# Kernel optimization log

Hardware: AMD Instinct MI355X
Metric: run time of the kernel (lower is better)

Reference implementation:

```python
import math
import jax, jax.numpy as jnp
import numpy as np

NUM_EXPERTS = 8
TOP_K = 2
CAPACITY_FACTOR = 1.0
B, S, H, I = 4, 2048, 1024, 4096


def setup_inputs() -> dict:
    key = jax.random.key(0)
    k_x, k_rw, k_wi, k_wo = jax.random.split(key, 4)
    x = jax.random.normal(k_x, (B, S, H), dtype=jnp.float32)
    # router: nn.Linear(H, E), xavier_uniform weight, zero-ish bias
    lim = math.sqrt(6.0 / (H + NUM_EXPERTS))
    router_w = jax.random.uniform(k_rw, (NUM_EXPERTS, H), minval=-lim, maxval=lim, dtype=jnp.float32)
    router_b = jnp.zeros((NUM_EXPERTS,), dtype=jnp.float32)
    # expert weights (scaled randn for numerical sanity)
    experts_inter = jax.random.normal(k_wi, (NUM_EXPERTS - 1, H, I), dtype=jnp.float32) / math.sqrt(H)
    experts_out = jax.random.normal(k_wo, (NUM_EXPERTS - 1, I, H), dtype=jnp.float32) / math.sqrt(I)
    return {"x": x, "router_w": router_w, "router_b": router_b,
            "experts_inter": experts_inter, "experts_out": experts_out}


def reference(x, router_w, router_b, experts_inter, experts_out):
    batch, seq, hidden = x.shape
    n_exp = router_w.shape[0]
    n_tok = batch * seq
    cap = math.ceil(n_tok / n_exp * CAPACITY_FACTOR)  # expert capacity

    # router: linear + softmax
    logits = jnp.einsum('bsh,eh->bse', x, router_w) + router_b
    weights_flat = jax.nn.softmax(logits, axis=-1).reshape(n_tok, n_exp)
    x_flat = x.reshape(n_tok, hidden)

    # top-k gating; scatter topk values back into a dense [N, E] matrix
    topk_vals, topk_idx = jax.lax.top_k(weights_flat, TOP_K)
    rows = jnp.arange(n_tok)[:, None]
    topk_flat = jnp.zeros_like(weights_flat).at[rows, topk_idx].set(topk_vals)
    routing_mask = (topk_flat > 0).astype(jnp.int32)

    # no-op path = last expert column (identity * gate weight)
    noop_w = topk_flat[:, -1]
    noop_mask = routing_mask[:, -1].astype(x.dtype)

    # real experts: columns 0..E-2; capacity-limited dispatch via per-column sort
    expert_w = topk_flat[:, :-1]           # [N, E-1]
    expert_mask = routing_mask[:, :-1]     # [N, E-1]
    sorted_indices = jnp.argsort(-expert_mask, axis=0)[:cap]          # [cap, E-1]
    sorted_mask = jnp.take_along_axis(expert_mask, sorted_indices, axis=0)
    used_idx = (sorted_indices * sorted_mask).reshape(-1)             # masked -> index 0

    inputs = x_flat[used_idx] * sorted_mask.reshape(-1).astype(x.dtype)[:, None]
    inputs = inputs.reshape(cap, n_exp - 1, hidden)                   # [cap, E-1, H]
    in_w = jnp.take_along_axis(expert_w, sorted_indices, axis=0)      # [cap, E-1]

    # batched per-expert FFN
    h = jax.nn.relu(jnp.einsum('ceh,ehi->cei', inputs, experts_inter))
    out = jnp.einsum('cei,eih->ceh', h, experts_out) * in_w[..., None]

    # scatter-combine (masked slots write zeros into row 0, harmless)
    combined = jnp.zeros_like(x_flat).at[used_idx].add(out.reshape(-1, hidden))
    combined = combined + x_flat * (noop_w * noop_mask)[:, None]
    return combined.reshape(batch, seq, hidden)
```

## Files before the change

kernel.cpp:

```cpp
#include <hip/hip_runtime.h>
#include <hip/hip_bf16.h>
#include <stdint.h>
#include <stddef.h>


#define N_TOK   8192
#define HDIM    1024
#define IDIM    4096
#define NEXP    7
#define CAP     1024

typedef __bf16 bf16_t;
typedef bf16_t bf16x8 __attribute__((ext_vector_type(8)));
typedef float  f32x4  __attribute__((ext_vector_type(4)));

typedef __attribute__((address_space(3))) char lds_char_t;
typedef __attribute__((address_space(1))) const char glob_char_t;

__device__ __forceinline__ void load_lds16(const void* g, void* l) {
    __builtin_amdgcn_global_load_lds((glob_char_t*)(uintptr_t)g,
                                     (lds_char_t*)(uintptr_t)l, 16, 0, 0);
}

__device__ __forceinline__ bf16x8 pack8(const float* v) {
    bf16x8 r;
#pragma unroll
    for (int j = 0; j < 8; j++) r[j] = (bf16_t)v[j];
    return r;
}

__global__ __launch_bounds__(256) void router_kernel(
    const float* __restrict__ x, const float* __restrict__ rw,
    const float* __restrict__ rb, float* __restrict__ routew)
{
    const int wave = threadIdx.x >> 6, lane = threadIdx.x & 63;
    const int t = blockIdx.x * 4 + wave;
    const float4* xr = (const float4*)(x + (size_t)t * HDIM);
    float4 xv[4];
#pragma unroll
    for (int r = 0; r < 4; r++) xv[r] = xr[lane + r * 64];
    float p[8];
#pragma unroll
    for (int e = 0; e < 8; e++) {
        const float4* wr = (const float4*)(rw + (size_t)e * HDIM);
        float s = 0.f;
#pragma unroll
        for (int r = 0; r < 4; r++) {
            float4 wv = wr[lane + r * 64];
            s += xv[r].x * wv.x + xv[r].y * wv.y + xv[r].z * wv.z + xv[r].w * wv.w;
        }
#pragma unroll
        for (int o = 32; o; o >>= 1) s += __shfl_xor(s, o, 64);
        p[e] = s + rb[e];
    }
    float m = p[0];
#pragma unroll
    for (int e = 1; e < 8; e++) m = fmaxf(m, p[e]);
    float sum = 0.f;
#pragma unroll
    for (int e = 0; e < 8; e++) { p[e] = expf(p[e] - m); sum += p[e]; }
    float inv = 1.f / sum;
#pragma unroll
    for (int e = 0; e < 8; e++) p[e] *= inv;
    int i1 = 0;
#pragma unroll
    for (int e = 1; e < 8; e++) if (p[e] > p[i1]) i1 = e;
    int i2 = (i1 == 0) ? 1 : 0;
#pragma unroll
    for (int e = 0; e < 8; e++) if (e != i1 && p[e] > p[i2]) i2 = e;
    if (lane == 0) {
#pragma unroll
        for (int c = 0; c < 8; c++)
            routew[(size_t)t * 8 + c] = (c == i1) ? p[i1] : ((c == i2) ? p[i2] : 0.f);
    }
}

__global__ __launch_bounds__(1024) void compact_kernel(
    const float* __restrict__ routew, int* __restrict__ list,
    float* __restrict__ wsel)
{
    const int e = blockIdx.x;
    const int tid = threadIdx.x, wave = tid >> 6, lane = tid & 63;
    for (int i = tid; i < CAP; i += 1024) { list[e * CAP + i] = -1; wsel[e * CAP + i] = 0.f; }
    __shared__ int cnt[16];
    __syncthreads();
    int base = 0;
    const unsigned long long below = (lane == 63) ? ~0ull >> 1 : ((1ull << lane) - 1);
    for (int chunk = 0; chunk < N_TOK / 1024; chunk++) {
        const int t = chunk * 1024 + tid;
        const float w = routew[(size_t)t * 8 + e];
        const bool sel = (w > 0.f);
        const unsigned long long mask = __ballot(sel);
        const int rnk = __popcll(mask & below);
        if (lane == 0) cnt[wave] = __popcll(mask);
        __syncthreads();
        int pre = base;
        for (int w2 = 0; w2 < wave; w2++) pre += cnt[w2];
        const int rank = pre + rnk;
        if (sel && rank < CAP) { list[e * CAP + rank] = t; wsel[e * CAP + rank] = w; }
        int tot = 0;
        for (int w2 = 0; w2 < 16; w2++) tot += cnt[w2];
        base += tot;
        __syncthreads();
    }
}

__global__ __launch_bounds__(128) void gather_kernel(
    const float* __restrict__ x, const int* __restrict__ list,
    bf16_t* __restrict__ A)
{
    const int row = blockIdx.x;
    const int t = list[row];
    const int i = threadIdx.x;
    float4 v0 = {0.f, 0.f, 0.f, 0.f}, v1 = v0;
    if (t >= 0) {
        const float4* xs = (const float4*)(x + (size_t)t * HDIM);
        v0 = xs[i * 2];
        v1 = xs[i * 2 + 1];
    }
    bf16x8 o;
    o[0] = (bf16_t)v0.x; o[1] = (bf16_t)v0.y; o[2] = (bf16_t)v0.z; o[3] = (bf16_t)v0.w;
    o[4] = (bf16_t)v1.x; o[5] = (bf16_t)v1.y; o[6] = (bf16_t)v1.z; o[7] = (bf16_t)v1.w;
    ((bf16x8*)(A + (size_t)row * HDIM))[i] = o;
}

__global__ __launch_bounds__(256) void initout_kernel(
    const float* __restrict__ x, const float* __restrict__ routew,
    float* __restrict__ out)
{
    const int t = blockIdx.x;
    const float c = routew[(size_t)t * 8 + 7];
    const float4* xs = (const float4*)(x + (size_t)t * HDIM);
    float4* o = (float4*)(out + (size_t)t * HDIM);
    float4 v = xs[threadIdx.x];
    v.x *= c; v.y *= c; v.z *= c; v.w *= c;
    o[threadIdx.x] = v;
}

template<int K, int N>
__global__ __launch_bounds__(256) void transpose_cvt(
    const float* __restrict__ W, bf16_t* __restrict__ Wt)
{
    __shared__ float Ts[64][65];
    const int t = threadIdx.x;
    const int e = blockIdx.z;
    const int ktile = blockIdx.y * 64, ntile = blockIdx.x * 64;
    const float* We = W + (size_t)e * K * N;
    const int kr = t >> 4, nc = (t & 15) * 4;
#pragma unroll
    for (int j = 0; j < 4; j++) {
        const float4 v = *(const float4*)(We + (size_t)(ktile + kr + j * 16) * N + ntile + nc);
        Ts[nc + 0][kr + j * 16] = v.x;
        Ts[nc + 1][kr + j * 16] = v.y;
        Ts[nc + 2][kr + j * 16] = v.z;
        Ts[nc + 3][kr + j * 16] = v.w;
    }
    __syncthreads();
    const int n = t >> 2, kc = (t & 3) * 16;
    bf16_t* o = Wt + ((size_t)e * N + ntile + n) * K + ktile + kc;
    bf16x8 p0, p1;
#pragma unroll
    for (int i = 0; i < 8; i++) {
        p0[i] = (bf16_t)Ts[n][kc + i];
        p1[i] = (bf16_t)Ts[n][kc + 8 + i];
    }
    ((bf16x8*)o)[0] = p0;
    ((bf16x8*)o)[1] = p1;
}

template<int KDIM, int NDIM, int KSPLIT, bool IS_G1>
__global__ __launch_bounds__(256) void ffn_gemm_t(
    const bf16_t* __restrict__ Ab, const bf16_t* __restrict__ Bt,
    bf16_t* __restrict__ Hout, const int* __restrict__ list,
    const float* __restrict__ wsel, float* __restrict__ out)
{
    constexpr int BM = 128, BN = 128, BK = 32;
    constexpr int KLEN = KDIM / KSPLIT;
    __shared__ __align__(16) bf16_t As[BM * BK];
    __shared__ __align__(16) bf16_t Bs[BN * BK];
    const int tid = threadIdx.x, wave = tid >> 6;
    const int lane = tid & 63;
    const int e = blockIdx.z / KSPLIT, ks = blockIdx.z % KSPLIT;
    const int mblk = blockIdx.y * BM, nblk = blockIdx.x * BN;

    const bf16_t* Ae = Ab + ((size_t)e * CAP + mblk) * KDIM + (size_t)ks * KLEN;
    const bf16_t* Be = Bt + ((size_t)e * NDIM + nblk) * KDIM + (size_t)ks * KLEN;

    const int r = tid >> 2, c = (tid & 3) * 8;
    const bf16_t* ag0 = Ae + (size_t)r * KDIM + c;
    const bf16_t* ag1 = ag0 + (size_t)64 * KDIM;
    const bf16_t* bg0 = Be + (size_t)r * KDIM + c;
    const bf16_t* bg1 = bg0 + (size_t)64 * KDIM;
    bf16_t* as0 = As + wave * 512;
    bf16_t* as1 = As + 2048 + wave * 512;
    bf16_t* bs0 = Bs + wave * 512;
    bf16_t* bs1 = Bs + 2048 + wave * 512;

    const int wm = (wave & 1) * 64, wn = (wave >> 1) * 64;
    const int lr = lane & 15, q = lane >> 4;

    f32x4 acc[4][4] = {};

    for (int k0 = 0; k0 < KLEN; k0 += BK) {
        load_lds16(ag0 + k0, as0);
        load_lds16(ag1 + k0, as1);
        load_lds16(bg0 + k0, bs0);
        load_lds16(bg1 + k0, bs1);
        __syncthreads();
        bf16x8 af[4], bfr[4];
#pragma unroll
        for (int i = 0; i < 4; i++)
            af[i] = *(const bf16x8*)(As + (wm + i * 16 + lr) * BK + q * 8);
#pragma unroll
        for (int j = 0; j < 4; j++)
            bfr[j] = *(const bf16x8*)(Bs + (wn + j * 16 + lr) * BK + q * 8);
#pragma unroll
        for (int i = 0; i < 4; i++)
#pragma unroll
            for (int j = 0; j < 4; j++)
                acc[i][j] = __builtin_amdgcn_mfma_f32_16x16x32_bf16(af[i], bfr[j], acc[i][j], 0, 0, 0);
        __syncthreads();
    }

    if (IS_G1) {
        bf16_t* Ho = Hout + ((size_t)e * CAP + mblk) * NDIM + nblk;
#pragma unroll
        for (int i = 0; i < 4; i++) {
            const int r0 = wm + i * 16 + q * 4;
#pragma unroll
            for (int reg = 0; reg < 4; reg++) {
                bf16_t* row = Ho + (size_t)(r0 + reg) * NDIM;
#pragma unroll
                for (int j = 0; j < 4; j++)
                    row[wn + j * 16 + lr] = (bf16_t)fmaxf(acc[i][j][reg], 0.f);
            }
        }
    } else {
#pragma unroll
        for (int i = 0; i < 4; i++) {
            const int r0 = mblk + wm + i * 16 + q * 4;
#pragma unroll
            for (int reg = 0; reg < 4; reg++) {
                const int row = r0 + reg;
                const int tok = list[e * CAP + row];
                const float wgt = wsel[e * CAP + row];
                if (tok >= 0) {
                    float* orow = out + (size_t)tok * NDIM + nblk;
#pragma unroll
                    for (int j = 0; j < 4; j++)
                        atomicAdd(orow + wn + j * 16 + lr, acc[i][j][reg] * wgt);
                }
            }
        }
    }
}

template<int KDIM, int NDIM, bool IS_G1>
__global__ __launch_bounds__(256) void ffn_gemm_fused(
    const bf16_t* __restrict__ Ab, const float* __restrict__ Wb,
    bf16_t* __restrict__ Hout, const int* __restrict__ list,
    const float* __restrict__ wsel, float* __restrict__ out)
{
    constexpr int BM = 128, BN = 128, BK = 32;
    __shared__ __align__(16) bf16_t As[BM * BK];
    __shared__ __align__(16) bf16_t Bs[BN * BK];
    const int tid = threadIdx.x, wave = tid >> 6, lane = tid & 63;
    const int e = blockIdx.z, mblk = blockIdx.y * BM, nblk = blockIdx.x * BN;

    const bf16_t* Ae = Ab + ((size_t)e * CAP + mblk) * KDIM;
    const float*  We = Wb + (size_t)e * KDIM * NDIM + nblk;

    const int ar = tid >> 2, ac = (tid & 3) * 8;
    const bf16_t* ag0 = Ae + (size_t)ar * KDIM + ac;
    const bf16_t* ag1 = ag0 + (size_t)64 * KDIM;
    bf16_t* as0 = As + wave * 512;
    bf16_t* as1 = As + 2048 + wave * 512;

    const int bn = tid & 127, bc = (tid >> 7) * 2;
    const float* bg = We + bn;
    bf16_t* bsw0 = Bs + bn * BK + ((bc ^ (bn & 3)) * 8);
    bf16_t* bsw1 = Bs + bn * BK + (((bc + 1) ^ (bn & 3)) * 8);

    const int wm = (wave & 1) * 64, wn = (wave >> 1) * 64;
    const int lr = lane & 15, q = lane >> 4;
    const int sw = q ^ ((wn + lr) & 3);

    f32x4 acc[4][4] = {};

    for (int k0 = 0; k0 < KDIM; k0 += BK) {
        load_lds16(ag0 + k0, as0);
        load_lds16(ag1 + k0, as1);
        const float* bp = bg + (size_t)(k0 + bc * 8) * NDIM;
        float v[16];
#pragma unroll
        for (int j = 0; j < 16; j++) v[j] = bp[(size_t)j * NDIM];
        bf16x8 p0 = pack8(v), p1 = pack8(v + 8);
        *(bf16x8*)bsw0 = p0;
        *(bf16x8*)bsw1 = p1;
        __syncthreads();
        bf16x8 af[4], bfr[4];
#pragma unroll
        for (int i = 0; i < 4; i++)
            af[i] = *(const bf16x8*)(As + (wm + i * 16 + lr) * BK + q * 8);
#pragma unroll
        for (int j = 0; j < 4; j++)
            bfr[j] = *(const bf16x8*)(Bs + (wn + j * 16 + lr) * BK + sw * 8);
#pragma unroll
        for (int i = 0; i < 4; i++)
#pragma unroll
            for (int j = 0; j < 4; j++)
                acc[i][j] = __builtin_amdgcn_mfma_f32_16x16x32_bf16(af[i], bfr[j], acc[i][j], 0, 0, 0);
        __syncthreads();
    }

    if (IS_G1) {
        bf16_t* Ho = Hout + ((size_t)e * CAP + mblk) * NDIM + nblk;
#pragma unroll
        for (int i = 0; i < 4; i++) {
            const int r0 = wm + i * 16 + q * 4;
#pragma unroll
            for (int reg = 0; reg < 4; reg++) {
                bf16_t* row = Ho + (size_t)(r0 + reg) * NDIM;
#pragma unroll
                for (int j = 0; j < 4; j++)
                    row[wn + j * 16 + lr] = (bf16_t)fmaxf(acc[i][j][reg], 0.f);
            }
        }
    } else {
#pragma unroll
        for (int i = 0; i < 4; i++) {
            const int r0 = mblk + wm + i * 16 + q * 4;
#pragma unroll
            for (int reg = 0; reg < 4; reg++) {
                const int row = r0 + reg;
                const int tok = list[e * CAP + row];
                const float wgt = wsel[e * CAP + row];
                if (tok >= 0) {
                    float* orow = out + (size_t)tok * NDIM + nblk;
#pragma unroll
                    for (int j = 0; j < 4; j++)
                        atomicAdd(orow + wn + j * 16 + lr, acc[i][j][reg] * wgt);
                }
            }
        }
    }
}

extern "C" void kernel_launch(void* const* d_in, const int* in_sizes, int n_in,
                              void* d_out, int out_size, void* d_ws, size_t ws_size,
                              hipStream_t stream) {
    const float* x  = (const float*)d_in[0];
    const float* rw = (const float*)d_in[1];
    const float* rb = (const float*)d_in[2];
    const float* w1 = (const float*)d_in[3];
    const float* w2 = (const float*)d_in[4];
    float* out = (float*)d_out;

    char* ws = (char*)d_ws;
    float*  routew = (float*)(ws);
    int*    list   = (int*)(ws + 262144);
    float*  wsel   = (float*)(ws + 262144 + 28672);
    bf16_t* Abuf   = (bf16_t*)(ws + 319488);
    bf16_t* Hbuf   = (bf16_t*)(ws + 14999552);
    bf16_t* Wt     = (bf16_t*)(ws + 73719808);

    const size_t NEED = 73719808ull + 58720256ull;

    router_kernel<<<N_TOK / 4, 256, 0, stream>>>(x, rw, rb, routew);
    compact_kernel<<<NEXP, 1024, 0, stream>>>(routew, list, wsel);
    gather_kernel<<<NEXP * CAP, 128, 0, stream>>>(x, list, Abuf);
    initout_kernel<<<N_TOK, 256, 0, stream>>>(x, routew, out);

    if (ws_size >= NEED) {
        transpose_cvt<HDIM, IDIM><<<dim3(IDIM / 64, HDIM / 64, NEXP), 256, 0, stream>>>(w1, Wt);
        ffn_gemm_t<HDIM, IDIM, 1, true><<<dim3(IDIM / 128, CAP / 128, NEXP), 256, 0, stream>>>(
            Abuf, Wt, Hbuf, nullptr, nullptr, nullptr);
        transpose_cvt<IDIM, HDIM><<<dim3(HDIM / 64, IDIM / 64, NEXP), 256, 0, stream>>>(w2, Wt);
        ffn_gemm_t<IDIM, HDIM, 2, false><<<dim3(HDIM / 128, CAP / 128, NEXP * 2), 256, 0, stream>>>(
            Hbuf, Wt, nullptr, list, wsel, out);
    } else {
        ffn_gemm_fused<HDIM, IDIM, true><<<dim3(IDIM / 128, CAP / 128, NEXP), 256, 0, stream>>>(
            Abuf, w1, Hbuf, nullptr, nullptr, nullptr);
        ffn_gemm_fused<IDIM, HDIM, false><<<dim3(HDIM / 128, CAP / 128, NEXP), 256, 0, stream>>>(
            Hbuf, w2, nullptr, list, wsel, out);
    }
}
```

Before: 551.7 us.

## Double-buffer GEMM LDS tiles with swizzle and fuse output init into router

The main expert GEMM now double-buffers its LDS tiles for A and B. It prefetches the next K tile with async global-to-LDS loads while MFMAs run on the current one, using explicit vmcnt waits and barriers. The LDS chunk layout is XOR-swizzled so fragment reads avoid bank conflicts. Separately, the no-op expert scaling of x into the output moves into the router kernel, which already holds x in registers, so the initout kernel and its extra read of x go away. The cost is twice the LDS per block, which may lower occupancy, plus hand-written wait and barrier sequencing that is easy to get wrong.

New measurement: 492.8 us. 10.7% less time.

```diff
diff --git a/kernel.cpp b/kernel.cpp
--- a/kernel.cpp
+++ b/kernel.cpp
@@ -31,7 +31,8 @@
 
 __global__ __launch_bounds__(256) void router_kernel(
     const float* __restrict__ x, const float* __restrict__ rw,
-    const float* __restrict__ rb, float* __restrict__ routew)
+    const float* __restrict__ rb, float* __restrict__ routew,
+    float* __restrict__ out)
 {
     const int wave = threadIdx.x >> 6, lane = threadIdx.x & 63;
     const int t = blockIdx.x * 4 + wave;
@@ -72,6 +73,14 @@
 #pragma unroll
         for (int c = 0; c < 8; c++)
             routew[(size_t)t * 8 + c] = (c == i1) ? p[i1] : ((c == i2) ? p[i2] : 0.f);
+    }
+    const float c7 = (i1 == 7 || i2 == 7) ? p[7] : 0.f;
+    float4* o = (float4*)(out + (size_t)t * HDIM);
+#pragma unroll
+    for (int r = 0; r < 4; r++) {
+        float4 v = xv[r];
+        v.x *= c7; v.y *= c7; v.z *= c7; v.w *= c7;
+        o[lane + r * 64] = v;
     }
 }
 
@@ -124,19 +133,6 @@
     ((bf16x8*)(A + (size_t)row * HDIM))[i] = o;
 }
 
-__global__ __launch_bounds__(256) void initout_kernel(
-    const float* __restrict__ x, const float* __restrict__ routew,
-    float* __restrict__ out)
-{
-    const int t = blockIdx.x;
-    const float c = routew[(size_t)t * 8 + 7];
-    const float4* xs = (const float4*)(x + (size_t)t * HDIM);
-    float4* o = (float4*)(out + (size_t)t * HDIM);
-    float4 v = xs[threadIdx.x];
-    v.x *= c; v.y *= c; v.z *= c; v.w *= c;
-    o[threadIdx.x] = v;
-}
-
 template<int K, int N>
 __global__ __launch_bounds__(256) void transpose_cvt(
     const float* __restrict__ W, bf16_t* __restrict__ Wt)
@@ -176,50 +172,65 @@
 {
     constexpr int BM = 128, BN = 128, BK = 32;
     constexpr int KLEN = KDIM / KSPLIT;
-    __shared__ __align__(16) bf16_t As[BM * BK];
-    __shared__ __align__(16) bf16_t Bs[BN * BK];
-    const int tid = threadIdx.x, wave = tid >> 6;
-    const int lane = tid & 63;
+    __shared__ __align__(16) bf16_t As[2][BM * BK];
+    __shared__ __align__(16) bf16_t Bs[2][BN * BK];
+    const int tid = threadIdx.x, wave = tid >> 6, lane = tid & 63;
     const int e = blockIdx.z / KSPLIT, ks = blockIdx.z % KSPLIT;
     const int mblk = blockIdx.y * BM, nblk = blockIdx.x * BN;
 
     const bf16_t* Ae = Ab + ((size_t)e * CAP + mblk) * KDIM + (size_t)ks * KLEN;
     const bf16_t* Be = Bt + ((size_t)e * NDIM + nblk) * KDIM + (size_t)ks * KLEN;
 
-    const int r = tid >> 2, c = (tid & 3) * 8;
-    const bf16_t* ag0 = Ae + (size_t)r * KDIM + c;
+    const int r = tid >> 2;
+    const int cc = tid & 3;
+    const int c = cc ^ ((r >> 1) & 3);
+    const bf16_t* ag0 = Ae + (size_t)r * KDIM + c * 8;
     const bf16_t* ag1 = ag0 + (size_t)64 * KDIM;
-    const bf16_t* bg0 = Be + (size_t)r * KDIM + c;
+    const bf16_t* bg0 = Be + (size_t)r * KDIM + c * 8;
     const bf16_t* bg1 = bg0 + (size_t)64 * KDIM;
-    bf16_t* as0 = As + wave * 512;
-    bf16_t* as1 = As + 2048 + wave * 512;
-    bf16_t* bs0 = Bs + wave * 512;
-    bf16_t* bs1 = Bs + 2048 + wave * 512;
+    const int woff = wave * 512;
 
     const int wm = (wave & 1) * 64, wn = (wave >> 1) * 64;
     const int lr = lane & 15, q = lane >> 4;
+    const int sw = (q ^ ((lr >> 1) & 3)) * 8;
 
     f32x4 acc[4][4] = {};
 
-    for (int k0 = 0; k0 < KLEN; k0 += BK) {
-        load_lds16(ag0 + k0, as0);
-        load_lds16(ag1 + k0, as1);
-        load_lds16(bg0 + k0, bs0);
-        load_lds16(bg1 + k0, bs1);
-        __syncthreads();
+    load_lds16(ag0, &As[0][woff]);
+    load_lds16(ag1, &As[0][2048 + woff]);
+    load_lds16(bg0, &Bs[0][woff]);
+    load_lds16(bg1, &Bs[0][2048 + woff]);
+
+    int p = 0;
+    for (int k0 = 0; k0 < KLEN; k0 += BK, p ^= 1) {
+        const bool more = (k0 + BK < KLEN);
+        if (more) {
+            const int kn = k0 + BK;
+            load_lds16(ag0 + kn, &As[p ^ 1][woff]);
+            load_lds16(ag1 + kn, &As[p ^ 1][2048 + woff]);
+            load_lds16(bg0 + kn, &Bs[p ^ 1][woff]);
+            load_lds16(bg1 + kn, &Bs[p ^ 1][2048 + woff]);
+            asm volatile("s_waitcnt vmcnt(4)" ::: "memory");
+        } else {
+            asm volatile("s_waitcnt vmcnt(0)" ::: "memory");
+        }
+        asm volatile("s_barrier" ::: "memory");
         bf16x8 af[4], bfr[4];
 #pragma unroll
         for (int i = 0; i < 4; i++)
-            af[i] = *(const bf16x8*)(As + (wm + i * 16 + lr) * BK + q * 8);
+            af[i] = *(const bf16x8*)(&As[p][(wm + i * 16 + lr) * BK + sw]);
 #pragma unroll
         for (int j = 0; j < 4; j++)
-            bfr[j] = *(const bf16x8*)(Bs + (wn + j * 16 + lr) * BK + q * 8);
+            bfr[j] = *(const bf16x8*)(&Bs[p][(wn + j * 16 + lr) * BK + sw]);
 #pragma unroll
         for (int i = 0; i < 4; i++)
 #pragma unroll
             for (int j = 0; j < 4; j++)
                 acc[i][j] = __builtin_amdgcn_mfma_f32_16x16x32_bf16(af[i], bfr[j], acc[i][j], 0, 0, 0);
-        __syncthreads();
+        if (more) {
+            asm volatile("s_waitcnt lgkmcnt(0)" ::: "memory");
+            asm volatile("s_barrier" ::: "memory");
+        }
     }
 
     if (IS_G1) {
@@ -283,7 +294,7 @@
 
     const int wm = (wave & 1) * 64, wn = (wave >> 1) * 64;
     const int lr = lane & 15, q = lane >> 4;
-    const int sw = q ^ ((wn + lr) & 3);
+    const int swz = q ^ ((wn + lr) & 3);
 
     f32x4 acc[4][4] = {};
 
@@ -304,7 +315,7 @@
             af[i] = *(const bf16x8*)(As + (wm + i * 16 + lr) * BK + q * 8);
 #pragma unroll
         for (int j = 0; j < 4; j++)
-            bfr[j] = *(const bf16x8*)(Bs + (wn + j * 16 + lr) * BK + sw * 8);
+            bfr[j] = *(const bf16x8*)(Bs + (wn + j * 16 + lr) * BK + swz * 8);
 #pragma unroll
         for (int i = 0; i < 4; i++)
 #pragma unroll
@@ -366,10 +377,9 @@
 
     const size_t NEED = 73719808ull + 58720256ull;
 
-    router_kernel<<<N_TOK / 4, 256, 0, stream>>>(x, rw, rb, routew);
+    router_kernel<<<N_TOK / 4, 256, 0, stream>>>(x, rw, rb, routew, out);
     compact_kernel<<<NEXP, 1024, 0, stream>>>(routew, list, wsel);
     gather_kernel<<<NEXP * CAP, 128, 0, stream>>>(x, list, Abuf);
-    initout_kernel<<<N_TOK, 256, 0, stream>>>(x, routew, out);
 
     if (ws_size >= NEED) {
         transpose_cvt<HDIM, IDIM><<<dim3(IDIM / 64, HDIM / 64, NEXP), 256, 0, stream>>>(w1, Wt);
```
